# Optimization experiments

Hardware: AMD Instinct MI355X
Metric: run time of the kernel (lower is better)

## Reference

```python
import jax, jax.numpy as jnp
import numpy as np


def _build_space_group(L):
    # C4v point group: rotations R^k and mirror*R^k, acting on Z_L^2 coords.
    R = np.array([[0, -1], [1, 0]])
    Mr = np.array([[1, 0], [0, -1]])
    mats = [np.linalg.matrix_power(R, k) for k in range(4)]
    mats += [Mr @ m for m in mats[:4]]
    mats = np.array(mats)  # (8,2,2)
    P = 8

    def find(A):
        for i in range(P):
            if np.array_equal(mats[i], A):
                return i
        raise ValueError('point group not closed')

    pcomp = np.array([[find(mats[a] @ mats[b]) for b in range(P)] for a in range(P)])
    pinv = np.array([find(np.round(np.linalg.inv(mats[a])).astype(int)) for a in range(P)])

    N = L * L
    G = P * N
    gx, gy = np.meshgrid(np.arange(L), np.arange(L), indexing='ij')
    coords = np.stack([gx.ravel(), gy.ravel()], -1)  # (N,2): site coords, also translation vecs

    # element g = p*N + (tx*L+ty) acts on coord v as  M_p v + t  (mod L)
    perms = np.zeros((G, N), np.int64)
    for p in range(P):
        w = coords @ mats[p].T  # (N,2)
        for t in range(N):
            u = (w + coords[t]) % L
            perms[p * N + t] = u[:, 0] * L + u[:, 1]

    pa = np.repeat(np.arange(P), N)  # point part per element
    ta = np.tile(coords, (P, 1))     # translation part per element
    mult = np.zeros((G, G), np.int64)
    for g in range(G):
        Ma = mats[pa[g]]
        pprod = pcomp[pa[g], pa]            # (G,)
        tprod = (ta @ Ma.T + ta[g]) % L     # (G,2): M_a t_b + t_a
        mult[g] = pprod * N + tprod[:, 0] * L + tprod[:, 1]
    inv = np.zeros((G,), np.int64)
    for g in range(G):
        Mi = mats[pinv[pa[g]]]
        ti = (-(Mi @ ta[g])) % L            # -M^{-1} t
        inv[g] = pinv[pa[g]] * N + ti[0] * L + ti[1]
    return perms, mult, inv


L_SIDE = 8
FEATS = (8, 8, 8)
BATCH = 1024


def setup_inputs() -> dict:
    perms, mult, inv = _build_space_group(L_SIDE)
    N = L_SIDE * L_SIDE
    G = perms.shape[0]
    c0, c1, c2 = FEATS
    ks = jax.random.split(jax.random.key(0), 8)
    s = jax.random.normal(ks[0], (BATCH, N), jnp.float32)
    # lecun_normal: std = 1/sqrt(fan_in)
    W_lift = jax.random.normal(ks[1], (N, c0), jnp.float32) / np.sqrt(N)
    b_lift = jnp.zeros((c0,), jnp.float32)
    K0 = jax.random.normal(ks[2], (G, c0, c1), jnp.float32) / np.sqrt(G * c0)
    K1 = jax.random.normal(ks[3], (G, c1, c2), jnp.float32) / np.sqrt(G * c1)
    W_amp = jax.random.normal(ks[4], (c2, 1), jnp.float32) / np.sqrt(c2)
    b_amp = jnp.zeros((1,), jnp.float32)
    W_ph = jnp.zeros((c2, 1), jnp.float32)  # zeros init as in module
    b_ph = jnp.zeros((1,), jnp.float32)
    return {'s': s, 'perms': jnp.asarray(perms), 'mult': jnp.asarray(mult),
            'inv': jnp.asarray(inv), 'W_lift': W_lift, 'b_lift': b_lift,
            'K0': K0, 'K1': K1, 'W_amp': W_amp, 'b_amp': b_amp,
            'W_ph': W_ph, 'b_ph': b_ph}


def reference(s, perms, mult, inv, W_lift, b_lift, K0, K1, W_amp, b_amp, W_ph, b_ph):
    G = perms.shape[0]
    s_g = s[:, perms].astype(jnp.float32)          # (B,G,N): lift gather
    x = jax.nn.gelu(s_g @ W_lift + b_lift)         # (B,G,c0)
    T = mult[:, inv]                                # (G,G): T[g,h] = g * h^{-1}
    scale = 1.0 / jnp.sqrt(jnp.asarray(G, jnp.float32))
    for K in (K0, K1):
        Kg = K[T]                                   # (G,G,cin,cout) regular-rep kernel gather
        x = jax.nn.gelu(jnp.einsum('bhc,ghcd->bgd', x, Kg) * scale)
    pooled = jnp.mean(x, axis=1)                    # trivial irrep: chi = 1/G
    amp = (pooled @ W_amp + b_amp)[..., 0]          # (B,)
    phase = (pooled @ W_ph + b_ph)[..., 0]
    return (amp + 1j * phase).astype(jnp.complex64)
```

## Files before the change

### kernel.cpp

```cpp
#include <hip/hip_runtime.h>
#include <hip/hip_bf16.h>
#include <cstdint>
#include <cstddef>

using s16x8 = __attribute__((ext_vector_type(8))) short;
using u16x8 = __attribute__((ext_vector_type(8))) unsigned short;
using f32x4 = __attribute__((ext_vector_type(4))) float;

#define GC 4096
#define SCALE_G 0.04419417382415922f

__device__ __forceinline__ float gelu_f(float x) {
  float u = 0.7978845608028654f * (x + 0.044715f * x * x * x);
  return 0.5f * x * (1.0f + tanhf(u));
}

__device__ __forceinline__ unsigned short f2bf(float f) {
  unsigned int u = __float_as_uint(f);
  unsigned int r = (u + 0x7fffu + ((u >> 16) & 1u)) >> 16;
  return (unsigned short)r;
}
__device__ __forceinline__ float bf2f(unsigned short b) {
  return __uint_as_float(((unsigned int)b) << 16);
}

__device__ __forceinline__ int idx_stride(const int* __restrict__ identity_row) {
  return (identity_row[1] == 0 && identity_row[3] == 0 && identity_row[5] == 0) ? 2 : 1;
}

typedef __attribute__((address_space(1))) void gvoid;
typedef __attribute__((address_space(3))) void lvoid;
__device__ __forceinline__ void gld16(const void* g, void* l) {
  __builtin_amdgcn_global_load_lds((gvoid*)g, (lvoid*)l, 16, 0, 0);
}

__device__ __forceinline__ s16x8 gload16(const unsigned short* p) {
  s16x8 r;
  asm volatile("global_load_dwordx4 %0, %1, off" : "=v"(r) : "v"(p));
  return r;
}

__global__ __launch_bounds__(256) void k_prep(
    const float* __restrict__ s, const int* __restrict__ perms,
    const int* __restrict__ mult, const int* __restrict__ inv,
    const float* __restrict__ Wl, const float* __restrict__ K0,
    const float* __restrict__ K1,
    unsigned short* __restrict__ sb, unsigned short* __restrict__ WPT,
    unsigned int* __restrict__ TallP, unsigned short* __restrict__ K0T0,
    unsigned short* __restrict__ K0T1) {
  const int tid = blockIdx.x * 256 + threadIdx.x;
  if (tid < 65536) {
    sb[tid] = f2bf(s[tid]);
  } else if (tid < 98304) {
    const int st = idx_stride(perms);
    const int t2 = tid - 65536;
    const int n = t2 & 63, h = t2 >> 6;
    const int m = perms[(size_t)t2 * st];
#pragma unroll
    for (int c = 0; c < 8; ++c)
      WPT[(size_t)((h << 3) + c) * 64 + m] = f2bf(Wl[n * 8 + c]);
  } else if (tid < 229376) {
    const int st = idx_stride(mult);
    const int i3 = tid - 98304;
    const int g = i3 & 511, w = i3 >> 9;
    const int h0 = (w >> 2) * 8 + (w & 3), h1 = h0 + 4;
    const int ih0 = inv[(size_t)h0 * st], ih1 = inv[(size_t)h1 * st];
    const unsigned int tv0 = (unsigned int)mult[(size_t)((g << 9) + ih0) * st];
    const unsigned int tv1 = (unsigned int)mult[(size_t)((g << 9) + ih1) * st];
    TallP[(size_t)w * 512 + g] = tv0 | (tv1 << 16);
  } else if (tid < 262144) {
    const int t4 = tid - 229376;
    const int tgh = t4 >> 6, e = t4 & 63, d = e >> 3, c = e & 7;
    K0T0[tgh * 64 + d * 8 + c] = f2bf(K0[tgh * 64 + c * 8 + d]);
  } else if (tid < 294912) {
    const int t5 = tid - 262144;
    const int tgh = t5 >> 6, e = t5 & 63, d = e >> 3, c = e & 7;
    K0T1[tgh * 64 + d * 8 + c] = f2bf(K1[tgh * 64 + c * 8 + d]);
  }
}

__global__ __launch_bounds__(256) void gemm_bf16(
    const unsigned short* __restrict__ A,
    const unsigned short* __restrict__ BT,
    unsigned short* __restrict__ C,
    const float* __restrict__ bias8,
    float scale, int M, int N, int K) {
  constexpr int BM = 64, BN = 128, BK = 64;
  __shared__ __align__(16) unsigned short As[3][BM * BK];
  __shared__ __align__(16) unsigned short Bs[3][BN * BK];

  const int nbm = M / BM;
  int bid = blockIdx.x;
  {
    const int q = (nbm * (N / BN)) >> 3;
    bid = (bid & 7) * q + (bid >> 3);
  }
  const int bn = bid / nbm, bm = bid % nbm;

  const int t = threadIdx.x;
  const int wid = t >> 6, lane = t & 63;
  const int wm = (wid >> 1) << 5;
  const int wn = (wid & 1) << 6;
  const int lr = lane & 15, lq = lane >> 4;

  const unsigned short* gA[2];
  const unsigned short* gB[4];
#pragma unroll
  for (int is = 0; is < 2; ++is) {
    const int sidx = is * 256 + t, row = sidx >> 3, c = (sidx & 7) ^ (row & 7);
    gA[is] = A + (size_t)(bm * BM + row) * K + c * 8;
  }
#pragma unroll
  for (int is = 0; is < 4; ++is) {
    const int sidx = is * 256 + t, row = sidx >> 3, c = (sidx & 7) ^ (row & 7);
    gB[is] = BT + (size_t)(bn * BN + row) * K + c * 8;
  }

  int aoff[2][2], boff[4][2];
#pragma unroll
  for (int i = 0; i < 2; ++i) {
    const int row = wm + i * 16 + lr;
#pragma unroll
    for (int ks = 0; ks < 2; ++ks)
      aoff[i][ks] = (row * 8 + ((ks * 4 + lq) ^ (row & 7))) * 16;
  }
#pragma unroll
  for (int j = 0; j < 4; ++j) {
    const int row = wn + j * 16 + lr;
#pragma unroll
    for (int ks = 0; ks < 2; ++ks)
      boff[j][ks] = (row * 8 + ((ks * 4 + lq) ^ (row & 7))) * 16;
  }

  auto stage = [&](int kt, int buf) {
    const int koff = kt * BK;
    char* la = (char*)&As[buf][0];
    char* lb = (char*)&Bs[buf][0];
#pragma unroll
    for (int is = 0; is < 2; ++is) gld16(gA[is] + koff, la + (is * 256 + t) * 16);
#pragma unroll
    for (int is = 0; is < 4; ++is) gld16(gB[is] + koff, lb + (is * 256 + t) * 16);
  };

  f32x4 acc[2][4] = {};
  const int nt = K / BK;
  stage(0, 0);
  if (nt > 1) stage(1, 1);

  int cur = 0;
  for (int kt = 0; kt < nt; ++kt) {
    if (kt < nt - 1) asm volatile("s_waitcnt vmcnt(6)" ::: "memory");
    else             asm volatile("s_waitcnt vmcnt(0)" ::: "memory");
    __builtin_amdgcn_s_barrier();
    asm volatile("" ::: "memory");
    __builtin_amdgcn_sched_barrier(0);
    if (kt + 2 < nt) {
      int nb = cur + 2; if (nb >= 3) nb -= 3;
      stage(kt + 2, nb);
    }
    const char* Ac = (const char*)&As[cur][0];
    const char* Bc = (const char*)&Bs[cur][0];
#pragma unroll
    for (int ks = 0; ks < 2; ++ks) {
      s16x8 a0 = *(const s16x8*)(Ac + aoff[0][ks]);
      s16x8 a1 = *(const s16x8*)(Ac + aoff[1][ks]);
      s16x8 b0 = *(const s16x8*)(Bc + boff[0][ks]);
      s16x8 b1 = *(const s16x8*)(Bc + boff[1][ks]);
      s16x8 b2 = *(const s16x8*)(Bc + boff[2][ks]);
      s16x8 b3 = *(const s16x8*)(Bc + boff[3][ks]);
      acc[0][0] = __builtin_amdgcn_mfma_f32_16x16x32_bf16(a0, b0, acc[0][0], 0, 0, 0);
      acc[0][1] = __builtin_amdgcn_mfma_f32_16x16x32_bf16(a0, b1, acc[0][1], 0, 0, 0);
      acc[0][2] = __builtin_amdgcn_mfma_f32_16x16x32_bf16(a0, b2, acc[0][2], 0, 0, 0);
      acc[0][3] = __builtin_amdgcn_mfma_f32_16x16x32_bf16(a0, b3, acc[0][3], 0, 0, 0);
      acc[1][0] = __builtin_amdgcn_mfma_f32_16x16x32_bf16(a1, b0, acc[1][0], 0, 0, 0);
      acc[1][1] = __builtin_amdgcn_mfma_f32_16x16x32_bf16(a1, b1, acc[1][1], 0, 0, 0);
      acc[1][2] = __builtin_amdgcn_mfma_f32_16x16x32_bf16(a1, b2, acc[1][2], 0, 0, 0);
      acc[1][3] = __builtin_amdgcn_mfma_f32_16x16x32_bf16(a1, b3, acc[1][3], 0, 0, 0);
    }
    cur = (cur == 2) ? 0 : cur + 1;
  }

#pragma unroll
  for (int i = 0; i < 2; ++i) {
    const int row0 = bm * BM + wm + i * 16 + lq * 4;
#pragma unroll
    for (int j = 0; j < 4; ++j) {
      const int col = bn * BN + wn + j * 16 + lr;
      const float bv = bias8 ? bias8[col & 7] : 0.0f;
#pragma unroll
      for (int r = 0; r < 4; ++r) {
        float v = gelu_f(acc[i][j][r] * scale + bv);
        C[(size_t)(row0 + r) * N + col] = f2bf(v);
      }
    }
  }
}

__global__ __launch_bounds__(512, 2) void gemm_fused(
    const unsigned short* __restrict__ A,
    const unsigned short* __restrict__ K0T,
    const unsigned int* __restrict__ TallP,
    unsigned short* __restrict__ C,
    float scale) {
  constexpr int Kdim = 4096, N = 4096, BM = 128, BK = 64, NT = Kdim / BK;
  __shared__ __align__(16) unsigned short As[3][BM * BK];
  __shared__ __align__(16) unsigned int TlP[64 * 4 * 16];

  const int bm = blockIdx.x & 7;
  const int bn = blockIdx.x >> 3;

  const int t = threadIdx.x;
  const int wid = t >> 6, lane = t & 63;
  const int wm = (wid >> 2) << 6;
  const int wn = (wid & 3) << 5;
  const int lr = lane & 15, lq = lane >> 4;
  const int glb = (wn >> 3) + (lr >> 3);
  const int dlo = lr & 7;

  const unsigned short* gA[2];
#pragma unroll
  for (int is = 0; is < 2; ++is) {
    const int sidx = is * 512 + t, row = sidx >> 3, c = (sidx & 7) ^ (row & 7);
    gA[is] = A + (size_t)(bm * BM + row) * Kdim + c * 8;
  }
  auto stage = [&](int kt, int buf) {
    const int koff = kt * BK;
    char* la = (char*)&As[buf][0];
#pragma unroll
    for (int is = 0; is < 2; ++is) gld16(gA[is] + koff, la + (is * 512 + t) * 16);
  };

  int aoff[4][2];
#pragma unroll
  for (int i = 0; i < 4; ++i) {
    const int row = wm + i * 16 + lr;
#pragma unroll
    for (int ks = 0; ks < 2; ++ks)
      aoff[i][ks] = (row * 8 + ((ks * 4 + lq) ^ (row & 7))) * 16;
  }

  stage(0, 0);
#pragma unroll
  for (int is = 0; is < 2; ++is) {
    const int sidx = is * 512 + t;
    const unsigned int* src = TallP + (size_t)(sidx >> 2) * 512 + bn * 16 + (sidx & 3) * 4;
    gld16(src, (char*)&TlP[0] + sidx * 16);
  }
  stage(1, 1);
  asm volatile("s_waitcnt vmcnt(2)" ::: "memory");
  __builtin_amdgcn_s_barrier();
  asm volatile("" ::: "memory");

  f32x4 acc[4][2] = {};
  s16x8 aE[4], aO[4];
  s16x8 bA[2][2], bB[2][2];
  unsigned int tvA[2], tvB[2];

  {
    unsigned int tv0[2];
#pragma unroll
    for (int j = 0; j < 2; ++j) tv0[j] = TlP[(0 * 4 + lq) * 16 + glb + j * 2];
#pragma unroll
    for (int j = 0; j < 2; ++j) tvA[j] = TlP[(1 * 4 + lq) * 16 + glb + j * 2];
#pragma unroll
    for (int j = 0; j < 2; ++j) {
      bA[j][0] = gload16(K0T + (tv0[j] & 0xFFFFu) * 64 + dlo * 8);
      bA[j][1] = gload16(K0T + (tv0[j] >> 16) * 64 + dlo * 8);
    }
    const char* Ac = (const char*)&As[0][0];
#pragma unroll
    for (int i = 0; i < 4; ++i) aE[i] = *(const s16x8*)(Ac + aoff[i][0]);
  }

  int cur = 0;
  auto iter = [&](int kt, s16x8 (&bu)[2][2], s16x8 (&bp)[2][2],
                  unsigned int (&tvu)[2], unsigned int (&tvn)[2]) {
    const char* Ac = (const char*)&As[cur][0];
    int nxt = cur + 1; if (nxt >= 3) nxt -= 3;
    const char* An = (const char*)&As[nxt][0];
    if (kt == 0 || kt == NT - 1) asm volatile("s_waitcnt vmcnt(0)" ::: "memory");
    else                         asm volatile("s_waitcnt vmcnt(2)" ::: "memory");
    __builtin_amdgcn_s_barrier();
    asm volatile("" ::: "memory");
    if (kt + 2 < NT) {
#pragma unroll
      for (int j = 0; j < 2; ++j)
        tvn[j] = TlP[((kt + 2) * 4 + lq) * 16 + glb + j * 2];
    }
#pragma unroll
    for (int i = 0; i < 4; ++i) aO[i] = *(const s16x8*)(Ac + aoff[i][1]);
    if (kt + 1 < NT) {
#pragma unroll
      for (int j = 0; j < 2; ++j) {
        bp[j][0] = gload16(K0T + (tvu[j] & 0xFFFFu) * 64 + dlo * 8);
        bp[j][1] = gload16(K0T + (tvu[j] >> 16) * 64 + dlo * 8);
      }
    }
    __builtin_amdgcn_sched_barrier(0);
    __builtin_amdgcn_s_setprio(1);
    acc[0][0] = __builtin_amdgcn_mfma_f32_16x16x32_bf16(aE[0], bu[0][0], acc[0][0], 0, 0, 0);
    acc[0][1] = __builtin_amdgcn_mfma_f32_16x16x32_bf16(aE[0], bu[1][0], acc[0][1], 0, 0, 0);
    acc[1][0] = __builtin_amdgcn_mfma_f32_16x16x32_bf16(aE[1], bu[0][0], acc[1][0], 0, 0, 0);
    acc[1][1] = __builtin_amdgcn_mfma_f32_16x16x32_bf16(aE[1], bu[1][0], acc[1][1], 0, 0, 0);
    acc[2][0] = __builtin_amdgcn_mfma_f32_16x16x32_bf16(aE[2], bu[0][0], acc[2][0], 0, 0, 0);
    acc[2][1] = __builtin_amdgcn_mfma_f32_16x16x32_bf16(aE[2], bu[1][0], acc[2][1], 0, 0, 0);
    acc[3][0] = __builtin_amdgcn_mfma_f32_16x16x32_bf16(aE[3], bu[0][0], acc[3][0], 0, 0, 0);
    acc[3][1] = __builtin_amdgcn_mfma_f32_16x16x32_bf16(aE[3], bu[1][0], acc[3][1], 0, 0, 0);
    __builtin_amdgcn_s_setprio(0);
    if (kt < NT - 1) asm volatile("s_waitcnt vmcnt(4)" ::: "memory");
    else             asm volatile("s_waitcnt vmcnt(0)" ::: "memory");
    __builtin_amdgcn_s_barrier();
    asm volatile("" ::: "memory");
    if (kt + 1 < NT) {
#pragma unroll
      for (int i = 0; i < 4; ++i) aE[i] = *(const s16x8*)(An + aoff[i][0]);
      if (kt + 2 < NT) {
        int nb = cur + 2; if (nb >= 3) nb -= 3;
        stage(kt + 2, nb);
      }
    }
    __builtin_amdgcn_sched_barrier(0);
    __builtin_amdgcn_s_setprio(1);
    acc[0][0] = __builtin_amdgcn_mfma_f32_16x16x32_bf16(aO[0], bu[0][1], acc[0][0], 0, 0, 0);
    acc[0][1] = __builtin_amdgcn_mfma_f32_16x16x32_bf16(aO[0], bu[1][1], acc[0][1], 0, 0, 0);
    acc[1][0] = __builtin_amdgcn_mfma_f32_16x16x32_bf16(aO[1], bu[0][1], acc[1][0], 0, 0, 0);
    acc[1][1] = __builtin_amdgcn_mfma_f32_16x16x32_bf16(aO[1], bu[1][1], acc[1][1], 0, 0, 0);
    acc[2][0] = __builtin_amdgcn_mfma_f32_16x16x32_bf16(aO[2], bu[0][1], acc[2][0], 0, 0, 0);
    acc[2][1] = __builtin_amdgcn_mfma_f32_16x16x32_bf16(aO[2], bu[1][1], acc[2][1], 0, 0, 0);
    acc[3][0] = __builtin_amdgcn_mfma_f32_16x16x32_bf16(aO[3], bu[0][1], acc[3][0], 0, 0, 0);
    acc[3][1] = __builtin_amdgcn_mfma_f32_16x16x32_bf16(aO[3], bu[1][1], acc[3][1], 0, 0, 0);
    __builtin_amdgcn_s_setprio(0);
    cur = nxt;
  };

  for (int kt2 = 0; kt2 < NT; kt2 += 2) {
    iter(kt2, bA, bB, tvA, tvB);
    iter(kt2 + 1, bB, bA, tvB, tvA);
  }

#pragma unroll
  for (int i = 0; i < 4; ++i) {
    const int row0 = bm * BM + wm + i * 16 + lq * 4;
#pragma unroll
    for (int j = 0; j < 2; ++j) {
      const int col = bn * 128 + wn + j * 16 + lr;
#pragma unroll
      for (int r = 0; r < 4; ++r) {
        float v = gelu_f(acc[i][j][r] * scale);
        C[(size_t)(row0 + r) * N + col] = f2bf(v);
      }
    }
  }
}


__global__ __launch_bounds__(256) void k_pool(const unsigned short* __restrict__ X3,
                                              float* __restrict__ pooled) {
  __shared__ float part[256];
  const int b = blockIdx.x, t = threadIdx.x;
  const unsigned short* row = X3 + (size_t)b * GC;
  float a = 0.f;
#pragma unroll
  for (int i = 0; i < 16; ++i) a += bf2f(row[t + 256 * i]);
  part[t] = a;
  __syncthreads();
  if (t < 8) {
    float s = 0.f;
    for (int k = 0; k < 32; ++k) s += part[t + 8 * k];
    pooled[b * 8 + t] = s * (1.0f / 512.0f);
  }
}

__global__ __launch_bounds__(256) void k_head(const float* __restrict__ pooled,
                                              const float* __restrict__ Wamp,
                                              const float* __restrict__ bamp,
                                              const float* __restrict__ Wph,
                                              const float* __restrict__ bph,
                                              float* __restrict__ out,
                                              int out_size) {
  int b = blockIdx.x * 256 + threadIdx.x;
  if (b >= 1024) return;
  float a = bamp[0], p = bph[0];
#pragma unroll
  for (int d = 0; d < 8; ++d) {
    float v = pooled[b * 8 + d];
    a += v * Wamp[d];
    p += v * Wph[d];
  }
  out[b] = a;
  if (out_size >= 2048) out[1024 + b] = p;
}


extern "C" void kernel_launch(void* const* d_in, const int* in_sizes, int n_in,
                              void* d_out, int out_size, void* d_ws, size_t ws_size,
                              hipStream_t stream) {
  (void)in_sizes; (void)n_in; (void)ws_size;
  const float* s    = (const float*)d_in[0];
  const int*   perms= (const int*)d_in[1];
  const int*   mult = (const int*)d_in[2];
  const int*   inv  = (const int*)d_in[3];
  const float* Wl   = (const float*)d_in[4];
  const float* bl   = (const float*)d_in[5];
  const float* K0   = (const float*)d_in[6];
  const float* K1   = (const float*)d_in[7];
  const float* Wamp = (const float*)d_in[8];
  const float* bamp = (const float*)d_in[9];
  const float* Wph  = (const float*)d_in[10];
  const float* bph  = (const float*)d_in[11];
  float* out = (float*)d_out;

  char* ws = (char*)d_ws;
  unsigned short* X1  = (unsigned short*)(ws);
  unsigned short* X2  = (unsigned short*)(ws + (8u << 20));
  unsigned short* X3  = X1;
  unsigned short* sb  = (unsigned short*)(ws + (16u << 20));
  unsigned short* WPT = (unsigned short*)(ws + (16u << 20) + (128u << 10));
  unsigned int*   TallP=(unsigned int*) (ws + (16u << 20) + (640u << 10));
  unsigned short* K0T0= (unsigned short*)(ws + (16u << 20) + (1152u << 10));
  unsigned short* K0T1= (unsigned short*)(ws + (16u << 20) + (1216u << 10));
  float* pooled       = (float*)(ws + (16u << 20) + (1280u << 10));

  k_prep<<<1152, 256, 0, stream>>>(s, perms, mult, inv, Wl, K0, K1,
                                   sb, WPT, TallP, K0T0, K0T1);
  gemm_bf16<<<512, 256, 0, stream>>>(sb, WPT, X1, bl, 1.0f, 1024, 4096, 64);
  gemm_fused<<<256, 512, 0, stream>>>(X1, K0T0, TallP, X2, SCALE_G);
  gemm_fused<<<256, 512, 0, stream>>>(X2, K0T1, TallP, X3, SCALE_G);
  k_pool<<<1024, 256, 0, stream>>>(X3, pooled);
  k_head<<<4, 256, 0, stream>>>(pooled, Wamp, bamp, Wph, bph, out, out_size);
}
```

Baseline: 115.2 us.

## Load A fragments directly from global into registers, dropping LDS staging and barriers

The fused gather GEMM no longer stages A tiles through a triple-buffered LDS ring with per-half-step barriers. Each wave now loads its A fragments straight from global memory into double-buffered registers, alongside the gathered K0T fragments, and waits with vmcnt counting only. This removes LDS traffic and workgroup barriers, but the four waves sharing a row band now each fetch the same A data (more global/L2 traffic), and register pressure rises.

Result: slower. 289.8 us (+151.7%).

```diff
diff --git a/kernel.cpp b/kernel.cpp
--- a/kernel.cpp
+++ b/kernel.cpp
@@ -202,8 +202,7 @@
     const unsigned int* __restrict__ TallP,
     unsigned short* __restrict__ C,
     float scale) {
-  constexpr int Kdim = 4096, N = 4096, BM = 128, BK = 64, NT = Kdim / BK;
-  __shared__ __align__(16) unsigned short As[3][BM * BK];
+  constexpr int Kdim = 4096, N = 4096, BM = 128, NT = 64;
   __shared__ __align__(16) unsigned int TlP[64 * 4 * 16];
 
   const int bm = blockIdx.x & 7;
@@ -217,42 +216,27 @@
   const int glb = (wn >> 3) + (lr >> 3);
   const int dlo = lr & 7;
 
-  const unsigned short* gA[2];
-#pragma unroll
-  for (int is = 0; is < 2; ++is) {
-    const int sidx = is * 512 + t, row = sidx >> 3, c = (sidx & 7) ^ (row & 7);
-    gA[is] = A + (size_t)(bm * BM + row) * Kdim + c * 8;
-  }
-  auto stage = [&](int kt, int buf) {
-    const int koff = kt * BK;
-    char* la = (char*)&As[buf][0];
-#pragma unroll
-    for (int is = 0; is < 2; ++is) gld16(gA[is] + koff, la + (is * 512 + t) * 16);
-  };
-
-  int aoff[4][2];
-#pragma unroll
-  for (int i = 0; i < 4; ++i) {
-    const int row = wm + i * 16 + lr;
+  const unsigned short* gAF[4][2];
+#pragma unroll
+  for (int i = 0; i < 4; ++i)
 #pragma unroll
     for (int ks = 0; ks < 2; ++ks)
-      aoff[i][ks] = (row * 8 + ((ks * 4 + lq) ^ (row & 7))) * 16;
-  }
-
-  stage(0, 0);
+      gAF[i][ks] = A + (size_t)(bm * BM + wm + i * 16 + lr) * Kdim +
+                   (ks * 4 + lq) * 8;
+
 #pragma unroll
   for (int is = 0; is < 2; ++is) {
     const int sidx = is * 512 + t;
-    const unsigned int* src = TallP + (size_t)(sidx >> 2) * 512 + bn * 16 + (sidx & 3) * 4;
+    const unsigned int* src =
+        TallP + (size_t)(sidx >> 2) * 512 + bn * 16 + (sidx & 3) * 4;
     gld16(src, (char*)&TlP[0] + sidx * 16);
   }
-  stage(1, 1);
-  asm volatile("s_waitcnt vmcnt(2)" ::: "memory");
+  asm volatile("s_waitcnt vmcnt(0)" ::: "memory");
   __builtin_amdgcn_s_barrier();
   asm volatile("" ::: "memory");
 
   f32x4 acc[4][2] = {};
-  s16x8 aE[4], aO[4];
+  s16x8 aA[4][2], aB[4][2];
   s16x8 bA[2][2], bB[2][2];
   unsigned int tvA[2], tvB[2];
 
@@ -262,80 +246,57 @@
     for (int j = 0; j < 2; ++j) tv0[j] = TlP[(0 * 4 + lq) * 16 + glb + j * 2];
 #pragma unroll
     for (int j = 0; j < 2; ++j) tvA[j] = TlP[(1 * 4 + lq) * 16 + glb + j * 2];
+#pragma unroll
+    for (int i = 0; i < 4; ++i)
+#pragma unroll
+      for (int ks = 0; ks < 2; ++ks) aA[i][ks] = gload16(gAF[i][ks]);
 #pragma unroll
     for (int j = 0; j < 2; ++j) {
       bA[j][0] = gload16(K0T + (tv0[j] & 0xFFFFu) * 64 + dlo * 8);
       bA[j][1] = gload16(K0T + (tv0[j] >> 16) * 64 + dlo * 8);
     }
-    const char* Ac = (const char*)&As[0][0];
-#pragma unroll
-    for (int i = 0; i < 4; ++i) aE[i] = *(const s16x8*)(Ac + aoff[i][0]);
-  }
-
-  int cur = 0;
-  auto iter = [&](int kt, s16x8 (&bu)[2][2], s16x8 (&bp)[2][2],
-                  unsigned int (&tvu)[2], unsigned int (&tvn)[2]) {
-    const char* Ac = (const char*)&As[cur][0];
-    int nxt = cur + 1; if (nxt >= 3) nxt -= 3;
-    const char* An = (const char*)&As[nxt][0];
-    if (kt == 0 || kt == NT - 1) asm volatile("s_waitcnt vmcnt(0)" ::: "memory");
-    else                         asm volatile("s_waitcnt vmcnt(2)" ::: "memory");
-    __builtin_amdgcn_s_barrier();
-    asm volatile("" ::: "memory");
+  }
+
+  auto iter = [&](int kt, s16x8 (&aC)[4][2], s16x8 (&aN)[4][2],
+                  s16x8 (&bC)[2][2], s16x8 (&bN)[2][2],
+                  unsigned int (&tvC)[2], unsigned int (&tvN)[2]) {
     if (kt + 2 < NT) {
 #pragma unroll
       for (int j = 0; j < 2; ++j)
-        tvn[j] = TlP[((kt + 2) * 4 + lq) * 16 + glb + j * 2];
-    }
-#pragma unroll
-    for (int i = 0; i < 4; ++i) aO[i] = *(const s16x8*)(Ac + aoff[i][1]);
+        tvN[j] = TlP[((kt + 2) * 4 + lq) * 16 + glb + j * 2];
+    }
     if (kt + 1 < NT) {
+      const int koff = (kt + 1) * 64;
+#pragma unroll
+      for (int i = 0; i < 4; ++i)
+#pragma unroll
+        for (int ks = 0; ks < 2; ++ks) aN[i][ks] = gload16(gAF[i][ks] + koff);
 #pragma unroll
       for (int j = 0; j < 2; ++j) {
-        bp[j][0] = gload16(K0T + (tvu[j] & 0xFFFFu) * 64 + dlo * 8);
-        bp[j][1] = gload16(K0T + (tvu[j] >> 16) * 64 + dlo * 8);
+        bN[j][0] = gload16(K0T + (tvC[j] & 0xFFFFu) * 64 + dlo * 8);
+        bN[j][1] = gload16(K0T + (tvC[j] >> 16) * 64 + dlo * 8);
       }
+      asm volatile("s_waitcnt vmcnt(12)" ::: "memory");
+    } else {
+      asm volatile("s_waitcnt vmcnt(0)" ::: "memory");
     }
     __builtin_amdgcn_sched_barrier(0);
     __builtin_amdgcn_s_setprio(1);
-    acc[0][0] = __builtin_amdgcn_mfma_f32_16x16x32_bf16(aE[0], bu[0][0], acc[0][0], 0, 0, 0);
-    acc[0][1] = __builtin_amdgcn_mfma_f32_16x16x32_bf16(aE[0], bu[1][0], acc[0][1], 0, 0, 0);
-    acc[1][0] = __builtin_amdgcn_mfma_f32_16x16x32_bf16(aE[1], bu[0][0], acc[1][0], 0, 0, 0);
-    acc[1][1] = __builtin_amdgcn_mfma_f32_16x16x32_bf16(aE[1], bu[1][0], acc[1][1], 0, 0, 0);
-    acc[2][0] = __builtin_amdgcn_mfma_f32_16x16x32_bf16(aE[2], bu[0][0], acc[2][0], 0, 0, 0);
-    acc[2][1] = __builtin_amdgcn_mfma_f32_16x16x32_bf16(aE[2], bu[1][0], acc[2][1], 0, 0, 0);
-    acc[3][0] = __builtin_amdgcn_mfma_f32_16x16x32_bf16(aE[3], bu[0][0], acc[3][0], 0, 0, 0);
-    acc[3][1] = __builtin_amdgcn_mfma_f32_16x16x32_bf16(aE[3], bu[1][0], acc[3][1], 0, 0, 0);
+#pragma unroll
+    for (int ks = 0; ks < 2; ++ks)
+#pragma unroll
+      for (int i = 0; i < 4; ++i) {
+        acc[i][0] = __builtin_amdgcn_mfma_f32_16x16x32_bf16(aC[i][ks], bC[0][ks],
+                                                            acc[i][0], 0, 0, 0);
+        acc[i][1] = __builtin_amdgcn_mfma_f32_16x16x32_bf16(aC[i][ks], bC[1][ks],
+                                                            acc[i][1], 0, 0, 0);
+      }
     __builtin_amdgcn_s_setprio(0);
-    if (kt < NT - 1) asm volatile("s_waitcnt vmcnt(4)" ::: "memory");
-    else             asm volatile("s_waitcnt vmcnt(0)" ::: "memory");
-    __builtin_amdgcn_s_barrier();
-    asm volatile("" ::: "memory");
-    if (kt + 1 < NT) {
-#pragma unroll
-      for (int i = 0; i < 4; ++i) aE[i] = *(const s16x8*)(An + aoff[i][0]);
-      if (kt + 2 < NT) {
-        int nb = cur + 2; if (nb >= 3) nb -= 3;
-        stage(kt + 2, nb);
-      }
-    }
-    __builtin_amdgcn_sched_barrier(0);
-    __builtin_amdgcn_s_setprio(1);
-    acc[0][0] = __builtin_amdgcn_mfma_f32_16x16x32_bf16(aO[0], bu[0][1], acc[0][0], 0, 0, 0);
-    acc[0][1] = __builtin_amdgcn_mfma_f32_16x16x32_bf16(aO[0], bu[1][1], acc[0][1], 0, 0, 0);
-    acc[1][0] = __builtin_amdgcn_mfma_f32_16x16x32_bf16(aO[1], bu[0][1], acc[1][0], 0, 0, 0);
-    acc[1][1] = __builtin_amdgcn_mfma_f32_16x16x32_bf16(aO[1], bu[1][1], acc[1][1], 0, 0, 0);
-    acc[2][0] = __builtin_amdgcn_mfma_f32_16x16x32_bf16(aO[2], bu[0][1], acc[2][0], 0, 0, 0);
-    acc[2][1] = __builtin_amdgcn_mfma_f32_16x16x32_bf16(aO[2], bu[1][1], acc[2][1], 0, 0, 0);
-    acc[3][0] = __builtin_amdgcn_mfma_f32_16x16x32_bf16(aO[3], bu[0][1], acc[3][0], 0, 0, 0);
-    acc[3][1] = __builtin_amdgcn_mfma_f32_16x16x32_bf16(aO[3], bu[1][1], acc[3][1], 0, 0, 0);
-    __builtin_amdgcn_s_setprio(0);
-    cur = nxt;
   };
 
   for (int kt2 = 0; kt2 < NT; kt2 += 2) {
-    iter(kt2, bA, bB, tvA, tvB);
-    iter(kt2 + 1, bB, bA, tvB, tvA);
+    iter(kt2,     aA, aB, bA, bB, tvA, tvB);
+    iter(kt2 + 1, aB, aA, bB, bA, tvB, tvA);
   }
 
 #pragma unroll
```
